# Performance work log

Measured on AMD Instinct MI355X. Metric: run time of the kernel, lower is better.

Reference implementation:

```python
import jax, jax.numpy as jnp
import numpy as np


def log_g(x):
    # log of g(x) = x+0.5 for x>=0, sigmoid(x) for x<0, computed stably
    return jnp.where(x >= 0, jnp.log(jax.nn.relu(x) + 0.5), -jax.nn.softplus(-x))


def setup_inputs() -> dict:
    key = jax.random.key(0)
    k1, k2 = jax.random.split(key)
    B, S, D = 4, 4096, 1024
    x = jax.random.normal(k1, (B, S, D), dtype=jnp.float32)
    W = jax.random.normal(k2, (D, 3 * D), dtype=jnp.float32) * (1.0 / np.sqrt(D))
    return {"x": x, "W": W}


def reference(x, W):
    # fused gate projection: [B,S,D] @ [D,3D] -> f_gate, i_gate, hidden
    gates = jnp.einsum('bsd,de->bse', x, W)
    f_gate, i_gate, hidden = jnp.split(gates, 3, axis=-1)

    # log-space normalized gates: log_f = log(sig(f)/(sig(f)+sig(i))) etc.
    diff = jax.nn.softplus(-f_gate) - jax.nn.softplus(-i_gate)
    log_f = -jax.nn.softplus(diff)
    log_i = -jax.nn.softplus(-diff)
    log_tilde_h = log_g(hidden)

    log_values = log_i + log_tilde_h
    # parallel scan in log space over seq axis (axis=1)
    a_star = jnp.cumsum(log_f, axis=1)
    log_h0_plus_b_star = jax.lax.cumlogsumexp(log_values - a_star, axis=1)
    h = jnp.exp(a_star + log_h0_plus_b_star)  # [B,S,D]
    return h  # to_out is Identity for expansion_factor == 1.0
```

## Files before the change

### kernel.cpp

```cpp
#include <hip/hip_runtime.h>
#include <hip/hip_fp16.h>
#include <cstdint>

typedef _Float16 half8  __attribute__((ext_vector_type(8)));
typedef _Float16 half4v __attribute__((ext_vector_type(4)));
typedef _Float16 half2v __attribute__((ext_vector_type(2)));
typedef float    floatx4 __attribute__((ext_vector_type(4)));

constexpr int Bb = 4, Ss = 4096, Dd = 1024;
constexpr int Mdim = Bb * Ss;
constexpr int Ndim = 3 * Dd;
constexpr int Kdim = Dd;
constexpr int CH = 256, LCH = Ss / CH;

__device__ __forceinline__ void gload_lds16(const void* g, void* l) {
  __builtin_amdgcn_global_load_lds(
      (const __attribute__((address_space(1))) uint32_t*)g,
      (__attribute__((address_space(3))) uint32_t*)l, 16, 0, 0);
}

__device__ __forceinline__ void gate_fv(float fg, float ig, float hg,
                                        float& fw, float& v) {
  float ef = __expf(fminf(-fg, 40.f));
  float ei = __expf(fminf(-ig, 40.f));
  float r  = __builtin_amdgcn_rcpf(2.f + ef + ei);
  fw = (1.f + ei) * r;
  float iw = (1.f + ef) * r;
  float g  = hg >= 0.f ? hg + 0.5f
                       : __builtin_amdgcn_rcpf(1.f + __expf(fminf(-hg, 40.f)));
  v = iw * g;
}

__global__ __launch_bounds__(256) void cvt_k(const float* __restrict__ X,
                                             _Float16* __restrict__ X16,
                                             const float* __restrict__ W,
                                             _Float16* __restrict__ WT) {
  __shared__ float tile[32][33];
  int bid = blockIdx.x;
  if (bid < 2048) {
    const int n4 = Mdim * Kdim / 4;
    for (int i = bid * 256 + threadIdx.x; i < n4; i += 2048 * 256) {
      float4 v = ((const float4*)X)[i];
      half4v o = {(_Float16)v.x, (_Float16)v.y, (_Float16)v.z, (_Float16)v.w};
      ((half4v*)X16)[i] = o;
    }
  } else {
    int b2 = bid - 2048;
    int tx = threadIdx.x & 31, ty = threadIdx.x >> 5;
    int n0 = (b2 % 96) * 32, k0 = (b2 / 96) * 32;
#pragma unroll
    for (int j = 0; j < 4; ++j) {
      int k = ty + j * 8;
      tile[k][tx] = W[(int64_t)(k0 + k) * Ndim + n0 + tx];
    }
    __syncthreads();
#pragma unroll
    for (int j = 0; j < 4; ++j) {
      int nl = ty + j * 8;
      int n = n0 + nl;
      int g = n >> 10, d = n & 1023;
      int p = (d >> 6) * 192 + g * 64 + (d & 63);
      WT[(int64_t)p * Kdim + k0 + tx] = (_Float16)tile[tx][nl];
    }
  }
}

constexpr int GBM = 256, GBN = 192, GBK = 64;
constexpr int NT = Kdim / GBK;
constexpr int LBUF = 57344;

__global__ __launch_bounds__(512, 2) void gemm8_k(const _Float16* __restrict__ A,
                                                  const _Float16* __restrict__ BT,
                                                  _Float16* __restrict__ fv) {
  extern __shared__ char lds[];
  const int tid = threadIdx.x;
  const int wid = tid >> 6, lane = tid & 63;
  const int wm = wid >> 2, wn = wid & 3;
  const int l15 = lane & 15, lq = lane >> 4;

  int wg = blockIdx.x;
  wg = (wg & 7) * 128 + (wg >> 3);
  const int m0 = (wg >> 4) * GBM;
  const int d0 = (wg & 15) * 64;

  int aO[4];
#pragma unroll
  for (int mi = 0; mi < 4; ++mi) {
    int r = wm * 64 + mi * 16 + l15;
    aO[mi] = r * 128 + ((lq ^ (r & 7)) << 4);
  }
  const int rB = wn * 16 + l15;
  const int bO = rB * 128 + ((lq ^ (rB & 7)) << 4);

  const int srr = (wid << 3) + (lane >> 3);
  const int ss = lane & 7;
  const _Float16* Abase = A + (size_t)m0 * Kdim;
  const _Float16* Bbase = BT + (size_t)(wg & 15) * 192 * Kdim;

  auto stage = [&](const _Float16* gsrc, int ldsBase, int nr) {
#pragma unroll
    for (int round = 0; round < 3; ++round) {
      if (round >= nr) break;
      int r = (round << 6) + srr;
      int c = ss ^ (r & 7);
      gload_lds16(gsrc + (size_t)r * Kdim + (c << 3),
                  lds + ldsBase + (round << 13) + (wid << 10));
    }
  };

  floatx4 acc[8][3] = {};

  stage(Abase, 0, 2);
  stage(Bbase, 32768, 3);
  stage(Abase + 128 * Kdim, 16384, 2);
  stage(Abase + 64, LBUF, 2);
  stage(Bbase + 64, LBUF + 32768, 3);
  asm volatile("s_waitcnt vmcnt(5)" ::: "memory");
  __builtin_amdgcn_s_barrier();

  for (int kt = 0; kt < NT; ++kt) {
    const int cur = (kt & 1) * LBUF, nxt = ((kt + 1) & 1) * LBUF;
    const _Float16* Akt1 = Abase + (kt + 1) * GBK;
    const _Float16* Akt2 = Abase + (kt + 2) * GBK;
    const _Float16* Bkt2 = Bbase + (kt + 2) * GBK;

    half8 a[4][2], b[3][2];

#pragma unroll
    for (int mi = 0; mi < 4; ++mi)
#pragma unroll
      for (int ks = 0; ks < 2; ++ks)
        a[mi][ks] = *(const half8*)(lds + cur + (aO[mi] ^ (ks << 6)));
#pragma unroll
    for (int g = 0; g < 3; ++g)
#pragma unroll
      for (int ks = 0; ks < 2; ++ks)
        b[g][ks] = *(const half8*)(lds + cur + 32768 + (g << 13) + (bO ^ (ks << 6)));
    if (kt + 1 < NT) stage(Akt1 + 128 * Kdim, nxt + 16384, 2);

    __builtin_amdgcn_s_setprio(1);
#pragma unroll
    for (int ks = 0; ks < 2; ++ks)
#pragma unroll
      for (int mi = 0; mi < 4; ++mi)
#pragma unroll
        for (int g = 0; g < 3; ++g)
          acc[mi][g] = __builtin_amdgcn_mfma_f32_16x16x32_f16(
              a[mi][ks], b[g][ks], acc[mi][g], 0, 0, 0);
    __builtin_amdgcn_s_setprio(0);

    __builtin_amdgcn_s_barrier();

#pragma unroll
    for (int mi = 0; mi < 4; ++mi)
#pragma unroll
      for (int ks = 0; ks < 2; ++ks)
        a[mi][ks] = *(const half8*)(lds + cur + 16384 + (aO[mi] ^ (ks << 6)));
    if (kt + 2 < NT) {
      stage(Akt2, cur, 2);
      stage(Bkt2, cur + 32768, 3);
    }

    __builtin_amdgcn_s_setprio(1);
#pragma unroll
    for (int ks = 0; ks < 2; ++ks)
#pragma unroll
      for (int mi = 0; mi < 4; ++mi)
#pragma unroll
        for (int g = 0; g < 3; ++g)
          acc[4 + mi][g] = __builtin_amdgcn_mfma_f32_16x16x32_f16(
              a[mi][ks], b[g][ks], acc[4 + mi][g], 0, 0, 0);
    __builtin_amdgcn_s_setprio(0);

    if (kt < NT - 2) {
      asm volatile("s_waitcnt vmcnt(5)" ::: "memory");
      __builtin_amdgcn_s_barrier();
    } else if (kt == NT - 2) {
      asm volatile("s_waitcnt vmcnt(0)" ::: "memory");
      __builtin_amdgcn_s_barrier();
    }
  }

  const int dcol = d0 + wn * 16 + l15;
#pragma unroll
  for (int hf = 0; hf < 2; ++hf)
#pragma unroll
    for (int mf = 0; mf < 4; ++mf) {
      int row = m0 + hf * 128 + wm * 64 + mf * 16 + (lq << 2);
#pragma unroll
      for (int r = 0; r < 4; ++r) {
        float fw, v;
        gate_fv(acc[hf * 4 + mf][0][r], acc[hf * 4 + mf][1][r],
                acc[hf * 4 + mf][2][r], fw, v);
        half2v o = {(_Float16)fw, (_Float16)v};
        *(half2v*)(fv + ((size_t)(row + r) * Dd + dcol) * 2) = o;
      }
    }
}

__global__ __launch_bounds__(256) void scan1_k(const _Float16* __restrict__ fv,
                                               float* __restrict__ Fc,
                                               float* __restrict__ Hc) {
  int d = threadIdx.x * 4;
  int c = blockIdx.y, b = blockIdx.z;
  const _Float16* p = fv + ((int64_t)(b * Ss + c * LCH) * Dd + d) * 2;
  float h[4] = {0.f, 0.f, 0.f, 0.f};
  float F[4] = {1.f, 1.f, 1.f, 1.f};
#pragma unroll 4
  for (int s = 0; s < LCH; ++s) {
    half8 q = *(const half8*)p;
#pragma unroll
    for (int j = 0; j < 4; ++j) {
      float fr = (float)q[2 * j], vr = (float)q[2 * j + 1];
      h[j] = fmaf(fr, h[j], vr);
      F[j] *= fr;
    }
    p += Dd * 2;
  }
  int co = (b * CH + c) * Dd + d;
  *(floatx4*)(Fc + co) = *(floatx4*)F;
  *(floatx4*)(Hc + co) = *(floatx4*)h;
}

__global__ __launch_bounds__(256) void scan2_k(const float* __restrict__ Fc,
                                               const float* __restrict__ Hc,
                                               float* __restrict__ Carry) {
  int idx = blockIdx.x * 256 + threadIdx.x;
  int b = idx >> 10, d = idx & (Dd - 1);
  float carry = 0.f;
#pragma unroll 8
  for (int c = 0; c < CH; ++c) {
    int co = (b * CH + c) * Dd + d;
    Carry[co] = carry;
    carry = fmaf(Fc[co], carry, Hc[co]);
  }
}

__global__ __launch_bounds__(256) void scan3_k(const _Float16* __restrict__ fv,
                                               const float* __restrict__ Carry,
                                               float* __restrict__ Out) {
  int d = threadIdx.x * 4;
  int c = blockIdx.y, b = blockIdx.z;
  int64_t m0 = (int64_t)(b * Ss + c * LCH);
  const _Float16* p = fv + (m0 * Dd + d) * 2;
  float* o = Out + m0 * Dd + d;
  int co = (b * CH + c) * Dd + d;
  floatx4 hv = *(const floatx4*)(Carry + co);
  float h[4] = {hv[0], hv[1], hv[2], hv[3]};
#pragma unroll 4
  for (int s = 0; s < LCH; ++s) {
    half8 q = *(const half8*)p;
#pragma unroll
    for (int j = 0; j < 4; ++j)
      h[j] = fmaf((float)q[2 * j], h[j], (float)q[2 * j + 1]);
    *(floatx4*)o = *(floatx4*)h;
    p += Dd * 2;
    o += Dd;
  }
}

extern "C" void kernel_launch(void* const* d_in, const int* in_sizes, int n_in,
                              void* d_out, int out_size, void* d_ws, size_t ws_size,
                              hipStream_t stream) {
  const float* x = (const float*)d_in[0];
  const float* W = (const float*)d_in[1];
  float* out = (float*)d_out;

  char* ws = (char*)d_ws;
  size_t off = 0;
  auto alloc = [&](size_t bytes) {
    char* p = ws + off;
    off += (bytes + 255) & ~size_t(255);
    return p;
  };
  _Float16* fv     = (_Float16*)alloc((size_t)Mdim * Dd * 2 * 2);
  float* Fc        = (float*)alloc((size_t)Bb * CH * Dd * 4);
  float* Hc        = (float*)alloc((size_t)Bb * CH * Dd * 4);
  float* Carry     = (float*)alloc((size_t)Bb * CH * Dd * 4);
  _Float16* x16    = (_Float16*)alloc((size_t)Mdim * Kdim * 2);
  _Float16* w16t   = (_Float16*)alloc((size_t)Ndim * Kdim * 2);
  if (off > ws_size) return;

  cvt_k<<<5120, 256, 0, stream>>>(x, x16, W, w16t);
  gemm8_k<<<dim3((Mdim / GBM) * (Dd / 64)), 512, 114688, stream>>>(x16, w16t, fv);
  scan1_k<<<dim3(1, CH, Bb), 256, 0, stream>>>(fv, Fc, Hc);
  scan2_k<<<(Bb * Dd) / 256, 256, 0, stream>>>(Fc, Hc, Carry);
  scan3_k<<<dim3(1, CH, Bb), 256, 0, stream>>>(fv, Carry, out);
}
```

Before: 183.3 us.

## Simplify GEMM double-buffer pipeline to one barrier per k-step

Replaces the staggered two-deep prefetch schedule, which issued half-tile loads at two points per iteration and used two barriers with partial vmcnt waits, with a plain double buffer. The whole next k-tile is issued at the top of the loop, all LDS fragments for both A halves are read before the MFMAs, and a full vmcnt(0) wait plus one barrier ends each iteration. This removes one barrier per iteration and keeps a single long MFMA run. In exchange the prefetch distance shrinks to one tile, register use grows because two A fragment sets are held, and the full drain each step can expose global load latency.

```diff
diff --git a/kernel.cpp b/kernel.cpp
--- a/kernel.cpp
+++ b/kernel.cpp
@@ -111,32 +111,38 @@
   floatx4 acc[8][3] = {};
 
   stage(Abase, 0, 2);
+  stage(Abase + 128 * Kdim, 16384, 2);
   stage(Bbase, 32768, 3);
-  stage(Abase + 128 * Kdim, 16384, 2);
-  stage(Abase + 64, LBUF, 2);
-  stage(Bbase + 64, LBUF + 32768, 3);
-  asm volatile("s_waitcnt vmcnt(5)" ::: "memory");
+  asm volatile("s_waitcnt vmcnt(0)" ::: "memory");
   __builtin_amdgcn_s_barrier();
 
   for (int kt = 0; kt < NT; ++kt) {
     const int cur = (kt & 1) * LBUF, nxt = ((kt + 1) & 1) * LBUF;
-    const _Float16* Akt1 = Abase + (kt + 1) * GBK;
-    const _Float16* Akt2 = Abase + (kt + 2) * GBK;
-    const _Float16* Bkt2 = Bbase + (kt + 2) * GBK;
-
-    half8 a[4][2], b[3][2];
-
+
+    if (kt + 1 < NT) {
+      const _Float16* Ak = Abase + (kt + 1) * GBK;
+      const _Float16* Bk = Bbase + (kt + 1) * GBK;
+      stage(Ak, nxt, 2);
+      stage(Ak + 128 * Kdim, nxt + 16384, 2);
+      stage(Bk, nxt + 32768, 3);
+    }
+
+    half8 a0[4][2], a1[4][2], b[3][2];
 #pragma unroll
     for (int mi = 0; mi < 4; ++mi)
 #pragma unroll
       for (int ks = 0; ks < 2; ++ks)
-        a[mi][ks] = *(const half8*)(lds + cur + (aO[mi] ^ (ks << 6)));
+        a0[mi][ks] = *(const half8*)(lds + cur + (aO[mi] ^ (ks << 6)));
 #pragma unroll
     for (int g = 0; g < 3; ++g)
 #pragma unroll
       for (int ks = 0; ks < 2; ++ks)
         b[g][ks] = *(const half8*)(lds + cur + 32768 + (g << 13) + (bO ^ (ks << 6)));
-    if (kt + 1 < NT) stage(Akt1 + 128 * Kdim, nxt + 16384, 2);
+#pragma unroll
+    for (int mi = 0; mi < 4; ++mi)
+#pragma unroll
+      for (int ks = 0; ks < 2; ++ks)
+        a1[mi][ks] = *(const half8*)(lds + cur + 16384 + (aO[mi] ^ (ks << 6)));
 
     __builtin_amdgcn_s_setprio(1);
 #pragma unroll
@@ -146,22 +152,7 @@
 #pragma unroll
         for (int g = 0; g < 3; ++g)
           acc[mi][g] = __builtin_amdgcn_mfma_f32_16x16x32_f16(
-              a[mi][ks], b[g][ks], acc[mi][g], 0, 0, 0);
-    __builtin_amdgcn_s_setprio(0);
-
-    __builtin_amdgcn_s_barrier();
-
-#pragma unroll
-    for (int mi = 0; mi < 4; ++mi)
-#pragma unroll
-      for (int ks = 0; ks < 2; ++ks)
-        a[mi][ks] = *(const half8*)(lds + cur + 16384 + (aO[mi] ^ (ks << 6)));
-    if (kt + 2 < NT) {
-      stage(Akt2, cur, 2);
-      stage(Bkt2, cur + 32768, 3);
-    }
-
-    __builtin_amdgcn_s_setprio(1);
+              a0[mi][ks], b[g][ks], acc[mi][g], 0, 0, 0);
 #pragma unroll
     for (int ks = 0; ks < 2; ++ks)
 #pragma unroll
@@ -169,13 +160,10 @@
 #pragma unroll
         for (int g = 0; g < 3; ++g)
           acc[4 + mi][g] = __builtin_amdgcn_mfma_f32_16x16x32_f16(
-              a[mi][ks], b[g][ks], acc[4 + mi][g], 0, 0, 0);
+              a1[mi][ks], b[g][ks], acc[4 + mi][g], 0, 0, 0);
     __builtin_amdgcn_s_setprio(0);
 
-    if (kt < NT - 2) {
-      asm volatile("s_waitcnt vmcnt(5)" ::: "memory");
-      __builtin_amdgcn_s_barrier();
-    } else if (kt == NT - 2) {
+    if (kt + 1 < NT) {
       asm volatile("s_waitcnt vmcnt(0)" ::: "memory");
       __builtin_amdgcn_s_barrier();
     }
```

Result: no change. 186.0 us (+1.5%).

## Fuse chunk-level scan reduction into GEMM epilogue, removing scan1 kernel

Applied to the files above, without the earlier changes.

The GEMM epilogue now computes each 16-row chunk's composed decay product and accumulated value. It does this in registers and through cross-lane shuffles, then writes the per-chunk carries straight to Fc/Hc. This removes the separate scan1 kernel, which re-read the whole fp16 fv buffer from memory. The cost is a few extra shuffles and FMAs in the GEMM epilogue, with some added register pressure there.

```diff
diff --git a/kernel.cpp b/kernel.cpp
--- a/kernel.cpp
+++ b/kernel.cpp
@@ -71,7 +71,9 @@
 
 __global__ __launch_bounds__(512, 2) void gemm8_k(const _Float16* __restrict__ A,
                                                   const _Float16* __restrict__ BT,
-                                                  _Float16* __restrict__ fv) {
+                                                  _Float16* __restrict__ fv,
+                                                  float* __restrict__ Fc,
+                                                  float* __restrict__ Hc) {
   extern __shared__ char lds[];
   const int tid = threadIdx.x;
   const int wid = tid >> 6, lane = tid & 63;
@@ -186,40 +188,34 @@
   for (int hf = 0; hf < 2; ++hf)
 #pragma unroll
     for (int mf = 0; mf < 4; ++mf) {
-      int row = m0 + hf * 128 + wm * 64 + mf * 16 + (lq << 2);
+      int row0 = m0 + hf * 128 + wm * 64 + mf * 16;
+      float Fl = 1.f, Hl = 0.f;
 #pragma unroll
       for (int r = 0; r < 4; ++r) {
         float fw, v;
         gate_fv(acc[hf * 4 + mf][0][r], acc[hf * 4 + mf][1][r],
                 acc[hf * 4 + mf][2][r], fw, v);
         half2v o = {(_Float16)fw, (_Float16)v};
-        *(half2v*)(fv + ((size_t)(row + r) * Dd + dcol) * 2) = o;
+        *(half2v*)(fv + ((size_t)(row0 + (lq << 2) + r) * Dd + dcol) * 2) = o;
+        float fr = (float)o[0], vr = (float)o[1];
+        Hl = fmaf(fr, Hl, vr);
+        Fl *= fr;
       }
-    }
-}
-
-__global__ __launch_bounds__(256) void scan1_k(const _Float16* __restrict__ fv,
-                                               float* __restrict__ Fc,
-                                               float* __restrict__ Hc) {
-  int d = threadIdx.x * 4;
-  int c = blockIdx.y, b = blockIdx.z;
-  const _Float16* p = fv + ((int64_t)(b * Ss + c * LCH) * Dd + d) * 2;
-  float h[4] = {0.f, 0.f, 0.f, 0.f};
-  float F[4] = {1.f, 1.f, 1.f, 1.f};
-#pragma unroll 4
-  for (int s = 0; s < LCH; ++s) {
-    half8 q = *(const half8*)p;
-#pragma unroll
-    for (int j = 0; j < 4; ++j) {
-      float fr = (float)q[2 * j], vr = (float)q[2 * j + 1];
-      h[j] = fmaf(fr, h[j], vr);
-      F[j] *= fr;
-    }
-    p += Dd * 2;
-  }
-  int co = (b * CH + c) * Dd + d;
-  *(floatx4*)(Fc + co) = *(floatx4*)F;
-  *(floatx4*)(Hc + co) = *(floatx4*)h;
+      float Fg = 1.f, Hg = 0.f;
+#pragma unroll
+      for (int j = 0; j < 4; ++j) {
+        float Fj = __shfl(Fl, j * 16 + l15);
+        float Hj = __shfl(Hl, j * 16 + l15);
+        Hg = fmaf(Fj, Hg, Hj);
+        Fg *= Fj;
+      }
+      if (lq == 0) {
+        int bb = row0 >> 12, s0 = row0 & (Ss - 1);
+        int co = (bb * CH + (s0 >> 4)) * Dd + dcol;
+        Fc[co] = Fg;
+        Hc[co] = Hg;
+      }
+    }
 }
 
 __global__ __launch_bounds__(256) void scan2_k(const float* __restrict__ Fc,
@@ -282,8 +278,7 @@
   if (off > ws_size) return;
 
   cvt_k<<<5120, 256, 0, stream>>>(x, x16, W, w16t);
-  gemm8_k<<<dim3((Mdim / GBM) * (Dd / 64)), 512, 114688, stream>>>(x16, w16t, fv);
-  scan1_k<<<dim3(1, CH, Bb), 256, 0, stream>>>(fv, Fc, Hc);
+  gemm8_k<<<dim3((Mdim / GBM) * (Dd / 64)), 512, 114688, stream>>>(x16, w16t, fv, Fc, Hc);
   scan2_k<<<(Bb * Dd) / 256, 256, 0, stream>>>(Fc, Hc, Carry);
   scan3_k<<<dim3(1, CH, Bb), 256, 0, stream>>>(fv, Carry, out);
 }
```

After: 180.1 us. Within noise of the previous version (-1.7%).
